# Kernel tuning notes

Measured on AMD Instinct MI355X. Metric: run time of the kernel, lower is better.

Reference implementation:

```python
import jax, jax.numpy as jnp
import numpy as np

NUM_HEADS = 16
ROPE_THETA = 10000.0


def setup_inputs() -> dict:
    key = jax.random.key(0)
    k1, k2, k3 = jax.random.split(key, 3)
    B, S, D = 2, 2048, 1024
    std_qkv = float(np.sqrt(2.0 / (D + 3 * D)))
    std_out = float(np.sqrt(2.0 / (D + D)))
    return {
        "x": jax.random.normal(k1, (B, S, D), dtype=jnp.float32),
        "qkv_w": jax.random.normal(k2, (3 * D, D), dtype=jnp.float32) * std_qkv,
        "out_w": jax.random.normal(k3, (D, D), dtype=jnp.float32) * std_out,
        "token_positions": jnp.arange(S, dtype=jnp.int32),
    }


def _apply_rope(x, token_positions, theta=ROPE_THETA):
    # x: [B, H, S, d_k], token_positions: [S]
    d_k = x.shape[-1]
    inv_freqs = 1.0 / (theta ** (jnp.arange(0, d_k, 2, dtype=jnp.float32) / d_k))  # [d_k/2]
    angles = token_positions.astype(jnp.float32)[:, None] * inv_freqs[None, :]     # [S, d_k/2]
    cos, sin = jnp.cos(angles), jnp.sin(angles)
    x_even, x_odd = x[..., 0::2], x[..., 1::2]
    r_even = x_even * cos - x_odd * sin
    r_odd = x_even * sin + x_odd * cos
    # interleave back: [..., d_k/2, 2] -> [..., d_k]
    return jnp.stack([r_even, r_odd], axis=-1).reshape(x.shape)


def reference(x, qkv_w, out_w, token_positions):
    B, S, D = x.shape
    H = NUM_HEADS
    d_k = D // H

    qkv = jnp.einsum("bsd,ed->bse", x, qkv_w)                  # [B, S, 3*D]
    qkv = qkv.reshape(B, S, 3, H, d_k)
    q, k, v = (jnp.transpose(qkv[:, :, i], (0, 2, 1, 3)) for i in range(3))  # each [B, H, S, d_k]

    q = _apply_rope(q, token_positions)
    k = _apply_rope(k, token_positions)

    scale = 1.0 / jnp.sqrt(jnp.asarray(d_k, dtype=x.dtype))
    scores = jnp.einsum("bhqd,bhkd->bhqk", q, k) * scale       # [B, H, S, S]
    causal = jnp.tril(jnp.ones((S, S), dtype=bool))
    scores = jnp.where(causal, scores, jnp.asarray(-jnp.inf, dtype=scores.dtype))
    attn = jax.nn.softmax(scores, axis=-1)
    out = jnp.einsum("bhqk,bhkd->bhqd", attn, v)               # [B, H, S, d_k]
    out = jnp.transpose(out, (0, 2, 1, 3)).reshape(B, S, D)    # [B, S, D]
    return jnp.einsum("bsd,ed->bse", out, out_w)               # [B, S, D]
```

## Files before the change

kernel.cpp:

```cpp
#include <hip/hip_runtime.h>

typedef __bf16 bf16x8 __attribute__((ext_vector_type(8)));
typedef float f32x4 __attribute__((ext_vector_type(4)));
typedef unsigned short u16;
typedef u16 u16x8 __attribute__((ext_vector_type(8)));
typedef u16 u16x2 __attribute__((ext_vector_type(2)));

__device__ __forceinline__ u16 f2bf(float f) {
    union { float f; unsigned u; } x; x.f = f;
    unsigned r = x.u + 0x7fffu + ((x.u >> 16) & 1u);
    return (u16)(r >> 16);
}
__device__ __forceinline__ float bf2f(u16 v) {
    union { unsigned u; float f; } x; x.u = ((unsigned)v) << 16;
    return x.f;
}
__device__ __forceinline__ bf16x8 as_bf16x8(u16x8 v) {
    return __builtin_bit_cast(bf16x8, v);
}
__device__ __forceinline__ void glds16(const void* g, void* l) {
    __builtin_amdgcn_global_load_lds(
        (const __attribute__((address_space(1))) void*)g,
        (__attribute__((address_space(3))) void*)l, 16, 0, 0);
}
__device__ __forceinline__ int swz(int r) { return (((r & 7) ^ ((r >> 3) & 7)) << 3); }

__global__ __launch_bounds__(256) void f32bf16(const float* __restrict__ in,
                                               u16* __restrict__ out, int n8) {
    int i = blockIdx.x * 256 + threadIdx.x;
    if (i >= n8) return;
    const float4* p = (const float4*)(in + (size_t)i * 8);
    float4 a = p[0], b = p[1];
    u16x8 o;
    o[0] = f2bf(a.x); o[1] = f2bf(a.y); o[2] = f2bf(a.z); o[3] = f2bf(a.w);
    o[4] = f2bf(b.x); o[5] = f2bf(b.y); o[6] = f2bf(b.z); o[7] = f2bf(b.w);
    *(u16x8*)(out + (size_t)i * 8) = o;
}

template<bool BF16OUT>
__global__ __launch_bounds__(256) void gemm128(const u16* __restrict__ A,
                                               const u16* __restrict__ B,
                                               void* __restrict__ Cv,
                                               int N, int K, int nbx) {
    __shared__ u16 As[2][4096];
    __shared__ u16 Bs[2][4096];
    const int tid = threadIdx.x, lane = tid & 63, wave = tid >> 6;
    const int cpx = gridDim.x >> 3;
    const int nid = (blockIdx.x & 7) * cpx + (blockIdx.x >> 3);
    const int m0 = (nid / nbx) << 7, n0 = (nid % nbx) << 7;
    const int wr = (wave >> 1) << 6, wc = (wave & 1) << 6;
    const int fr = lane & 15, fo = (lane >> 4) << 3;
    const int srow = tid >> 2, scol = (tid & 3) << 3;
    const u16* Ag = A + (size_t)(m0 + srow) * K + scol;
    const u16* Bg = B + (size_t)(n0 + srow) * K + scol;
    u16* AsW = &As[0][0] + (wave << 9);
    u16* BsW = &Bs[0][0] + (wave << 9);
    f32x4 acc[4][4] = {};
    const int nsteps = K >> 5;
    glds16(Ag, AsW);
    glds16(Ag + (size_t)64 * K, AsW + 2048);
    glds16(Bg, BsW);
    glds16(Bg + (size_t)64 * K, BsW + 2048);
    int cur = 0;
    for (int s = 0; s < nsteps; ++s) {
        __syncthreads();
        if (s + 1 < nsteps) {
            const u16* Ap = Ag + (s + 1) * 32;
            const u16* Bp = Bg + (s + 1) * 32;
            const int nb = (cur ^ 1) << 12;
            glds16(Ap, AsW + nb);
            glds16(Ap + (size_t)64 * K, AsW + nb + 2048);
            glds16(Bp, BsW + nb);
            glds16(Bp + (size_t)64 * K, BsW + nb + 2048);
        }
        const u16* Ab = &As[cur][0];
        const u16* Bb = &Bs[cur][0];
        bf16x8 af[4], bfr[4];
        #pragma unroll
        for (int i = 0; i < 4; ++i)
            af[i] = *(const bf16x8*)(Ab + (wr + i * 16 + fr) * 32 + fo);
        #pragma unroll
        for (int i = 0; i < 4; ++i)
            bfr[i] = *(const bf16x8*)(Bb + (wc + i * 16 + fr) * 32 + fo);
        #pragma unroll
        for (int i = 0; i < 4; ++i)
            #pragma unroll
            for (int j = 0; j < 4; ++j)
                acc[i][j] = __builtin_amdgcn_mfma_f32_16x16x32_bf16(af[i], bfr[j], acc[i][j], 0, 0, 0);
        cur ^= 1;
    }
    const int cr = (lane >> 4) << 2, cc = lane & 15;
    if constexpr (BF16OUT) {
        u16* C = (u16*)Cv;
        #pragma unroll
        for (int i = 0; i < 4; ++i)
            for (int j = 0; j < 4; ++j)
                for (int r = 0; r < 4; ++r)
                    C[(size_t)(m0 + wr + i * 16 + cr + r) * N + (n0 + wc + j * 16 + cc)] =
                        f2bf(acc[i][j][r]);
    } else {
        float* C = (float*)Cv;
        #pragma unroll
        for (int i = 0; i < 4; ++i)
            for (int j = 0; j < 4; ++j)
                for (int r = 0; r < 4; ++r)
                    C[(size_t)(m0 + wr + i * 16 + cr + r) * N + (n0 + wc + j * 16 + cc)] =
                        acc[i][j][r];
    }
}

__global__ __launch_bounds__(256) void rope_split(const u16* __restrict__ qkv,
                                                  const int* __restrict__ pos,
                                                  u16* __restrict__ Qb,
                                                  u16* __restrict__ Kb) {
    int tid = blockIdx.x * 256 + threadIdx.x;
    int t = tid & 31;
    int h = (tid >> 5) & 15;
    int s = (tid >> 9) & 2047;
    int b = tid >> 20;
    const u16* row = qkv + (size_t)((b << 11) + s) * 3072;
    float fp  = (float)pos[s];
    float inv = exp2f((float)t * -0.4152410118609203f);
    float rev = fp * inv * 0.15915494309189535f;
    rev = rev - floorf(rev);
    float sn = __builtin_amdgcn_sinf(rev);
    float cs = __builtin_amdgcn_cosf(rev);
    int off = h * 64 + 2 * t;
    u16x2 q2 = *(const u16x2*)(row + off);
    u16x2 k2 = *(const u16x2*)(row + 1024 + off);
    float qx = bf2f(q2[0]), qy = bf2f(q2[1]);
    float kx = bf2f(k2[0]), ky = bf2f(k2[1]);
    size_t oidx = (((size_t)(b * 16 + h) * 2048) + s) * 64 + 2 * t;
    const float qs = 0.18033688011112042f;
    u16x2 qo, ko;
    qo[0] = f2bf((qx * cs - qy * sn) * qs);
    qo[1] = f2bf((qx * sn + qy * cs) * qs);
    ko[0] = f2bf(kx * cs - ky * sn);
    ko[1] = f2bf(ky * cs + kx * sn);
    *(u16x2*)&Qb[oidx] = qo;
    *(u16x2*)&Kb[oidx] = ko;
}

__global__ __launch_bounds__(256) void vtrans(const u16* __restrict__ qkv,
                                              u16* __restrict__ Vt) {
    __shared__ u16 lds[64][72];
    const int t = threadIdx.x;
    const int st = blockIdx.x, h = blockIdx.y, b = blockIdx.z;
    const int s0 = st << 6;
    {
        const int r = t >> 2, c0 = (t & 3) << 4;
        const u16* src = qkv + (size_t)((b << 11) + s0 + r) * 3072 + 2048 + h * 64 + c0;
        *(u16x8*)&lds[r][c0]     = *(const u16x8*)src;
        *(u16x8*)&lds[r][c0 + 8] = *(const u16x8*)(src + 8);
    }
    __syncthreads();
    const size_t obase = ((size_t)((b << 4) + h) << 17) + (st << 6);
    #pragma unroll
    for (int w = 0; w < 2; ++w) {
        const int q = t + (w << 8);
        const int d = q >> 3, c = q & 7;
        u16x8 o;
        #pragma unroll
        for (int i = 0; i < 8; ++i) {
            const int p = (c << 3) + i;
            const int k = ((p >> 5) << 5) + (((p >> 3) & 3) << 2) + (p & 3)
                        + (((p >> 2) & 1) << 4);
            o[i] = lds[k][d];
        }
        *(u16x8*)(Vt + obase + ((size_t)d << 11) + (c << 3)) = o;
    }
}

__global__ __launch_bounds__(512, 4) void attn_causal(const u16* __restrict__ Q,
                                                      const u16* __restrict__ K,
                                                      const u16* __restrict__ Vt,
                                                      u16* __restrict__ O) {
    __shared__ u16 smem[16384];
    __shared__ float cmb[5120];
    const int tid = threadIdx.x, lane = tid & 63, wave = tid >> 6;
    const int nid = ((blockIdx.x & 7) << 6) + (blockIdx.x >> 3);
    const int pr = nid & 15, h = (nid >> 4) & 15, b = nid >> 8;
    const int S = 2048;
    const size_t base = (size_t)((b << 4) + h) << 17;
    const int fr = lane & 15, fo = (lane >> 4) << 3, cr = (lane >> 4) << 2;
    const int schk = lane & 7, srow8 = lane >> 3;
    const int qsub = wave >> 1, half = wave & 1;
    float* const slot = cmb + qsub * 1280 + lane * 20;
    u16x8 ones_u;
    #pragma unroll
    for (int i = 0; i < 8; ++i) ones_u[i] = 0x3F80;
    const bf16x8 ones = as_bf16x8(ones_u);

    auto stage = [&](int t, int bi) {
        const int r  = (wave << 3) + srow8;
        const int ck = (schk ^ srow8 ^ wave) << 3;
        glds16(K  + base + ((size_t)((t << 6) + r) << 6) + ck,
               &smem[(bi << 12) + (wave << 9)]);
        glds16(Vt + base + ((size_t)r << 11) + (t << 6) + ck,
               &smem[8192 + (bi << 12) + (wave << 9)]);
    };

    for (int phase = 0; phase < 2; ++phase) {
        const int qt = phase ? (31 - pr) : pr;
        const int nkt = qt + 1;
        const int qw = (qt << 6) + (qsub << 4);
        bf16x8 aq0, aq1;
        {
            const u16* qrow = Q + base + (size_t)(qw + fr) * 64;
            aq0 = as_bf16x8(*(const u16x8*)(qrow + fo));
            aq1 = as_bf16x8(*(const u16x8*)(qrow + 32 + fo));
        }
        f32x4 oacc[4] = {};
        f32x4 lacc = {};
        const int qloc = (qsub << 4) + fr;
        stage(0, 0);
        for (int t = 0; t < nkt; ++t) {
            __syncthreads();
            if (t + 1 < nkt) stage(t + 1, (t + 1) & 1);
            const u16* Kb = smem + ((t & 1) << 12);
            const u16* Vb = smem + 8192 + ((t & 1) << 12);
            const bool diag = (t == nkt - 1);
            f32x4 sacc[2];
            #pragma unroll
            for (int ch = 0; ch < 2; ++ch) {
                const int r = ((half << 1) + ch) * 16 + fr;
                const int sw = swz(r);
                bf16x8 bk0 = *(const bf16x8*)&Kb[r * 64 + (fo ^ sw)];
                bf16x8 bk1 = *(const bf16x8*)&Kb[r * 64 + ((32 + fo) ^ sw)];
                f32x4 sc = {};
                sc = __builtin_amdgcn_mfma_f32_16x16x32_bf16(bk0, aq0, sc, 0, 0, 0);
                sc = __builtin_amdgcn_mfma_f32_16x16x32_bf16(bk1, aq1, sc, 0, 0, 0);
                sacc[ch] = sc;
            }
            bf16x8 pa;
            #pragma unroll
            for (int ch = 0; ch < 2; ++ch) {
                const int cglob = (half << 1) + ch;
                #pragma unroll
                for (int r = 0; r < 4; ++r) {
                    float e = exp2f(sacc[ch][r]);
                    if (diag) {
                        const int kloc = (cglob << 4) + cr + r;
                        e = (kloc <= qloc) ? e : 0.f;
                    }
                    pa[ch * 4 + r] = (__bf16)e;
                }
            }
            lacc = __builtin_amdgcn_mfma_f32_16x16x32_bf16(pa, ones, lacc, 0, 0, 0);
            #pragma unroll
            for (int tt = 0; tt < 4; ++tt) {
                const int d = tt * 16 + fr;
                bf16x8 bv = *(const bf16x8*)&Vb[d * 64 + (((half << 5) + fo) ^ swz(d))];
                oacc[tt] = __builtin_amdgcn_mfma_f32_16x16x32_bf16(pa, bv, oacc[tt], 0, 0, 0);
            }
        }
        __syncthreads();
        if (half) {
            #pragma unroll
            for (int tt = 0; tt < 4; ++tt) *(f32x4*)(slot + tt * 4) = oacc[tt];
            *(f32x4*)(slot + 16) = lacc;
        }
        __syncthreads();
        if (!half) {
            #pragma unroll
            for (int tt = 0; tt < 4; ++tt) oacc[tt] += *(const f32x4*)(slot + tt * 4);
            lacc += *(const f32x4*)(slot + 16);
            f32x4 inv;
            #pragma unroll
            for (int j = 0; j < 4; ++j) inv[j] = 1.f / lacc[j];
            #pragma unroll
            for (int tt = 0; tt < 4; ++tt)
                for (int j = 0; j < 4; ++j)
                    O[(size_t)(b * S + qw + cr + j) * 1024 + h * 64 + tt * 16 + fr] =
                        f2bf(oacc[tt][j] * inv[j]);
        }
        __syncthreads();
    }
}

extern "C" void kernel_launch(void* const* d_in, const int* in_sizes, int n_in,
                              void* d_out, int out_size, void* d_ws, size_t ws_size,
                              hipStream_t stream) {
    const float* x     = (const float*)d_in[0];
    const float* qkv_w = (const float*)d_in[1];
    const float* out_w = (const float*)d_in[2];
    const int*   pos   = (const int*)d_in[3];
    float* out = (float*)d_out;

    char* ws = (char*)d_ws;
    u16* qkv16 = (u16*)ws;
    u16* Qb    = (u16*)(ws + 25165824);
    u16* Kb    = (u16*)(ws + 33554432);
    u16* Vtg   = (u16*)(ws + 41943040);
    u16* x16   = (u16*)(ws + 50331648);
    u16* att16 = (u16*)(ws + 50331648);
    u16* w16   = (u16*)(ws + 58720256);
    u16* ow16  = (u16*)(ws + 65011712);

    f32bf16<<<2048, 256, 0, stream>>>(x, x16, 524288);
    f32bf16<<<1536, 256, 0, stream>>>(qkv_w, w16, 393216);
    f32bf16<<<512, 256, 0, stream>>>(out_w, ow16, 131072);
    gemm128<true><<<768, 256, 0, stream>>>(x16, w16, (void*)qkv16, 3072, 1024, 24);
    rope_split<<<8192, 256, 0, stream>>>(qkv16, pos, Qb, Kb);
    vtrans<<<dim3(32, 16, 2), 256, 0, stream>>>(qkv16, Vtg);
    attn_causal<<<512, 512, 0, stream>>>(Qb, Kb, Vtg, att16);
    gemm128<false><<<256, 256, 0, stream>>>(att16, ow16, (void*)out, 1024, 1024, 8);
}
```

Before: 121.8 us.

## Load K/V fragments directly from global into registers, drop LDS staging

```diff
diff --git a/kernel.cpp b/kernel.cpp
--- a/kernel.cpp
+++ b/kernel.cpp
@@ -23,7 +23,6 @@
         (const __attribute__((address_space(1))) void*)g,
         (__attribute__((address_space(3))) void*)l, 16, 0, 0);
 }
-__device__ __forceinline__ int swz(int r) { return (((r & 7) ^ ((r >> 3) & 7)) << 3); }
 
 __global__ __launch_bounds__(256) void f32bf16(const float* __restrict__ in,
                                                u16* __restrict__ out, int n8) {
@@ -175,7 +174,6 @@
                                                       const u16* __restrict__ K,
                                                       const u16* __restrict__ Vt,
                                                       u16* __restrict__ O) {
-    __shared__ u16 smem[16384];
     __shared__ float cmb[5120];
     const int tid = threadIdx.x, lane = tid & 63, wave = tid >> 6;
     const int nid = ((blockIdx.x & 7) << 6) + (blockIdx.x >> 3);
@@ -183,7 +181,6 @@
     const int S = 2048;
     const size_t base = (size_t)((b << 4) + h) << 17;
     const int fr = lane & 15, fo = (lane >> 4) << 3, cr = (lane >> 4) << 2;
-    const int schk = lane & 7, srow8 = lane >> 3;
     const int qsub = wave >> 1, half = wave & 1;
     float* const slot = cmb + qsub * 1280 + lane * 20;
     u16x8 ones_u;
@@ -191,14 +188,12 @@
     for (int i = 0; i < 8; ++i) ones_u[i] = 0x3F80;
     const bf16x8 ones = as_bf16x8(ones_u);
 
-    auto stage = [&](int t, int bi) {
-        const int r  = (wave << 3) + srow8;
-        const int ck = (schk ^ srow8 ^ wave) << 3;
-        glds16(K  + base + ((size_t)((t << 6) + r) << 6) + ck,
-               &smem[(bi << 12) + (wave << 9)]);
-        glds16(Vt + base + ((size_t)r << 11) + (t << 6) + ck,
-               &smem[8192 + (bi << 12) + (wave << 9)]);
-    };
+    const u16* const Kp0 = K + base + (size_t)(((half << 1) + 0) * 16 + fr) * 64 + fo;
+    const u16* const Kp1 = K + base + (size_t)(((half << 1) + 1) * 16 + fr) * 64 + fo;
+    const u16* const Vp0 = Vt + base + (size_t)(0 * 16 + fr) * 2048 + (half << 5) + fo;
+    const u16* const Vp1 = Vt + base + (size_t)(1 * 16 + fr) * 2048 + (half << 5) + fo;
+    const u16* const Vp2 = Vt + base + (size_t)(2 * 16 + fr) * 2048 + (half << 5) + fo;
+    const u16* const Vp3 = Vt + base + (size_t)(3 * 16 + fr) * 2048 + (half << 5) + fo;
 
     for (int phase = 0; phase < 2; ++phase) {
         const int qt = phase ? (31 - pr) : pr;
@@ -213,47 +208,57 @@
         f32x4 oacc[4] = {};
         f32x4 lacc = {};
         const int qloc = (qsub << 4) + fr;
-        stage(0, 0);
-        for (int t = 0; t < nkt; ++t) {
-            __syncthreads();
-            if (t + 1 < nkt) stage(t + 1, (t + 1) & 1);
-            const u16* Kb = smem + ((t & 1) << 12);
-            const u16* Vb = smem + 8192 + ((t & 1) << 12);
+
+        auto loadK = [&](int t, u16x8& a, u16x8& b, u16x8& c, u16x8& d) {
+            const size_t to = (size_t)t << 12;
+            a = *(const u16x8*)(Kp0 + to);
+            b = *(const u16x8*)(Kp0 + to + 32);
+            c = *(const u16x8*)(Kp1 + to);
+            d = *(const u16x8*)(Kp1 + to + 32);
+        };
+        auto tile = [&](int t, u16x8 k00, u16x8 k01, u16x8 k10, u16x8 k11) {
             const bool diag = (t == nkt - 1);
-            f32x4 sacc[2];
-            #pragma unroll
-            for (int ch = 0; ch < 2; ++ch) {
-                const int r = ((half << 1) + ch) * 16 + fr;
-                const int sw = swz(r);
-                bf16x8 bk0 = *(const bf16x8*)&Kb[r * 64 + (fo ^ sw)];
-                bf16x8 bk1 = *(const bf16x8*)&Kb[r * 64 + ((32 + fo) ^ sw)];
-                f32x4 sc = {};
-                sc = __builtin_amdgcn_mfma_f32_16x16x32_bf16(bk0, aq0, sc, 0, 0, 0);
-                sc = __builtin_amdgcn_mfma_f32_16x16x32_bf16(bk1, aq1, sc, 0, 0, 0);
-                sacc[ch] = sc;
-            }
+            const size_t vo = (size_t)t << 6;
+            u16x8 v0 = *(const u16x8*)(Vp0 + vo);
+            u16x8 v1 = *(const u16x8*)(Vp1 + vo);
+            u16x8 v2 = *(const u16x8*)(Vp2 + vo);
+            u16x8 v3 = *(const u16x8*)(Vp3 + vo);
+            f32x4 s0 = {}, s1 = {};
+            s0 = __builtin_amdgcn_mfma_f32_16x16x32_bf16(as_bf16x8(k00), aq0, s0, 0, 0, 0);
+            s0 = __builtin_amdgcn_mfma_f32_16x16x32_bf16(as_bf16x8(k01), aq1, s0, 0, 0, 0);
+            s1 = __builtin_amdgcn_mfma_f32_16x16x32_bf16(as_bf16x8(k10), aq0, s1, 0, 0, 0);
+            s1 = __builtin_amdgcn_mfma_f32_16x16x32_bf16(as_bf16x8(k11), aq1, s1, 0, 0, 0);
             bf16x8 pa;
             #pragma unroll
-            for (int ch = 0; ch < 2; ++ch) {
-                const int cglob = (half << 1) + ch;
-                #pragma unroll
-                for (int r = 0; r < 4; ++r) {
-                    float e = exp2f(sacc[ch][r]);
-                    if (diag) {
-                        const int kloc = (cglob << 4) + cr + r;
-                        e = (kloc <= qloc) ? e : 0.f;
-                    }
-                    pa[ch * 4 + r] = (__bf16)e;
+            for (int r = 0; r < 4; ++r) {
+                float e0 = exp2f(s0[r]);
+                float e1 = exp2f(s1[r]);
+                if (diag) {
+                    const int k0l = ((half << 1) << 4) + cr + r;
+                    const int k1l = k0l + 16;
+                    e0 = (k0l <= qloc) ? e0 : 0.f;
+                    e1 = (k1l <= qloc) ? e1 : 0.f;
                 }
+                pa[r]     = (__bf16)e0;
+                pa[4 + r] = (__bf16)e1;
             }
             lacc = __builtin_amdgcn_mfma_f32_16x16x32_bf16(pa, ones, lacc, 0, 0, 0);
-            #pragma unroll
-            for (int tt = 0; tt < 4; ++tt) {
-                const int d = tt * 16 + fr;
-                bf16x8 bv = *(const bf16x8*)&Vb[d * 64 + (((half << 5) + fo) ^ swz(d))];
-                oacc[tt] = __builtin_amdgcn_mfma_f32_16x16x32_bf16(pa, bv, oacc[tt], 0, 0, 0);
-            }
-        }
+            oacc[0] = __builtin_amdgcn_mfma_f32_16x16x32_bf16(pa, as_bf16x8(v0), oacc[0], 0, 0, 0);
+            oacc[1] = __builtin_amdgcn_mfma_f32_16x16x32_bf16(pa, as_bf16x8(v1), oacc[1], 0, 0, 0);
+            oacc[2] = __builtin_amdgcn_mfma_f32_16x16x32_bf16(pa, as_bf16x8(v2), oacc[2], 0, 0, 0);
+            oacc[3] = __builtin_amdgcn_mfma_f32_16x16x32_bf16(pa, as_bf16x8(v3), oacc[3], 0, 0, 0);
+        };
+
+        u16x8 a0, a1, a2, a3, b0, b1, b2, b3;
+        loadK(0, a0, a1, a2, a3);
+        for (int t = 0; t < nkt; t += 2) {
+            if (t + 1 < nkt) loadK(t + 1, b0, b1, b2, b3);
+            tile(t, a0, a1, a2, a3);
+            if (t + 1 >= nkt) break;
+            if (t + 2 < nkt) loadK(t + 2, a0, a1, a2, a3);
+            tile(t + 1, b0, b1, b2, b3);
+        }
+
         __syncthreads();
         if (half) {
             #pragma unroll
```

Result: slower. 202.0 us (+65.8%).
